# Kernel tuning notes

Measured on AMD Instinct MI355X. Metric: run time of the kernel, lower is better.

## Reference

```python
import jax, jax.numpy as jnp
import numpy as np

DIM = 1024
NUM_HEADS = 16
HEAD_DIM = DIM // NUM_HEADS
ROPE_BASE = 10000.0


def _rope_cos_sin(seq_len, head_dim, dtype):
    inv_freq = 1.0 / (ROPE_BASE ** (jnp.arange(0, head_dim, 2, dtype=jnp.float32) / head_dim))
    t = jnp.arange(seq_len, dtype=jnp.float32)
    freqs = jnp.einsum('i,j->ij', t, inv_freq)          # (S, head_dim/2)
    emb = jnp.concatenate([freqs, freqs], axis=-1)       # (S, head_dim)
    return jnp.cos(emb).astype(dtype), jnp.sin(emb).astype(dtype)


def _rotate_half(x):
    x1, x2 = jnp.split(x, 2, axis=-1)
    return jnp.concatenate([-x2, x1], axis=-1)


def setup_inputs() -> dict:
    key = jax.random.key(0)
    k1, k2, k3 = jax.random.split(key, 3)
    B, S = 2, 2048
    x = jax.random.normal(k1, (B, S, DIM), dtype=jnp.float32)
    w_qkv = jax.random.normal(k2, (3 * DIM, DIM), dtype=jnp.float32) * (DIM ** -0.5)
    w_out = jax.random.normal(k3, (DIM, DIM), dtype=jnp.float32) * (DIM ** -0.5)
    return {"x": x, "w_qkv": w_qkv, "w_out": w_out}


def reference(x, w_qkv, w_out):
    B, S, _ = x.shape
    scale = HEAD_DIM ** -0.5

    qkv = jnp.einsum('bsd,ed->bse', x, w_qkv)                 # (B, S, 3*DIM)
    qkv = qkv.reshape(B, S, 3, NUM_HEADS, HEAD_DIM)
    qkv = jnp.transpose(qkv, (2, 0, 3, 1, 4))                  # (3, B, H, S, hd)
    Q, K, V = qkv[0], qkv[1], qkv[2]

    cos, sin = _rope_cos_sin(S, HEAD_DIM, x.dtype)             # (S, hd)
    Q = Q * cos + _rotate_half(Q) * sin
    K = K * cos + _rotate_half(K) * sin

    scores = jnp.einsum('bhqd,bhkd->bhqk', Q, K) * scale       # (B, H, S, S)
    causal = jnp.tril(jnp.ones((S, S), dtype=bool))
    scores = jnp.where(causal[None, None], scores, jnp.asarray(-1e9, scores.dtype))
    attn = jax.nn.softmax(scores, axis=-1)

    out = jnp.einsum('bhqk,bhkd->bhqd', attn, V)               # (B, H, S, hd)
    out = jnp.transpose(out, (0, 2, 1, 3)).reshape(B, S, DIM)
    out = jnp.einsum('bsd,ed->bse', out, w_out)
    return out
```

## Files before the change

### kernel.cpp

```cpp
#include <hip/hip_runtime.h>
#include <hip/hip_bf16.h>

#define DIM 1024
#define NHEADS 16
#define HD 64
#define BB 2
#define SS 2048
#define MTOT (BB*SS)
#define SCALE 0.125f
#define QSCALE 0.1803368801111204f

typedef __attribute__((ext_vector_type(8))) short bf16x8;
typedef __attribute__((ext_vector_type(4))) float f32x4;

__device__ __forceinline__ float bf2f(short u) {
  union { float f; unsigned int i; } v;
  v.i = ((unsigned int)(unsigned short)u) << 16;
  return v.f;
}
__device__ __forceinline__ short f2bf(float f) {
  union { float f; unsigned int i; } v; v.f = f;
  unsigned int r = v.i + 0x7fffu + ((v.i >> 16) & 1u);
  return (short)(r >> 16);
}
__device__ __forceinline__ unsigned int cvtpk_bf16(float lo, float hi) {
  unsigned int r;
  asm("v_cvt_pk_bf16_f32 %0, %1, %2" : "=v"(r) : "v"(lo), "v"(hi));
  return r;
}
__device__ __forceinline__ void async_load16(const short* g, short* l) {
  __builtin_amdgcn_global_load_lds(
      (const __attribute__((address_space(1))) unsigned int*)g,
      (__attribute__((address_space(3))) unsigned int*)l, 16, 0, 0);
}

__global__ void cvt3_kernel(const float* __restrict__ a, short* __restrict__ oa, int na,
                            const float* __restrict__ b, short* __restrict__ ob, int nb,
                            const float* __restrict__ c, short* __restrict__ oc, int nc) {
  int stride = gridDim.x * blockDim.x;
  int tot = na + nb + nc;
  for (int q = blockIdx.x * blockDim.x + threadIdx.x; q < tot; q += stride) {
    const float* src; short* dst; int off;
    if (q < na)            { src = a; dst = oa; off = q; }
    else if (q < na + nb)  { src = b; dst = ob; off = q - na; }
    else                   { src = c; dst = oc; off = q - na - nb; }
    float4 v = *(const float4*)(src + (size_t)off * 4);
    short4 o;
    o.x = f2bf(v.x); o.y = f2bf(v.y); o.z = f2bf(v.z); o.w = f2bf(v.w);
    *(short4*)(dst + (size_t)off * 4) = o;
  }
}

__global__ void rope_table_kernel(float* __restrict__ ct, float* __restrict__ st) {
  int i = blockIdx.x * blockDim.x + threadIdx.x;
  if (i >= SS * 32) return;
  int s = i >> 5, j = i & 31;
  float inv = 1.0f / powf(10000.0f, (float)(2 * j) / 64.0f);
  float ang = (float)s * inv;
  ct[i] = cosf(ang);
  st[i] = sinf(ang);
}

template<bool OUT_F32>
__global__ __launch_bounds__(256) void gemm_bt(
    const short* __restrict__ A, const short* __restrict__ B,
    void* __restrict__ C, int M, int N, int K) {
  __shared__ __align__(16) short As[128][32];
  __shared__ __align__(16) short Bs[128][32];
  const int nbx = N >> 7;
  const int chunk = gridDim.x >> 3;
  const int wg = (blockIdx.x & 7) * chunk + (blockIdx.x >> 3);
  const int m0 = (wg / nbx) * 128, n0 = (wg % nbx) * 128;
  const int tid = threadIdx.x;
  const int lane = tid & 63;
  const int wid = tid >> 6;
  const int wm = (wid >> 1) * 64, wn = (wid & 1) * 64;
  const int row = lane & 15, kg = (lane >> 4) * 8;
  const int lrow = lane >> 2;
  const int lcol = (lane & 3) * 8;

  f32x4 acc[4][4];
#pragma unroll
  for (int m = 0; m < 4; m++)
#pragma unroll
    for (int n = 0; n < 4; n++) acc[m][n] = (f32x4){0.f, 0.f, 0.f, 0.f};

  for (int kk = 0; kk < K; kk += 32) {
    __syncthreads();
#pragma unroll
    for (int i = 0; i < 2; i++) {
      int base = i * 64 + wid * 16;
      async_load16(A + (size_t)(m0 + base + lrow) * K + kk + lcol, &As[base][0]);
      async_load16(B + (size_t)(n0 + base + lrow) * K + kk + lcol, &Bs[base][0]);
    }
    __syncthreads();
    bf16x8 af[4], bfr[4];
#pragma unroll
    for (int m = 0; m < 4; m++) af[m] = *(const bf16x8*)(&As[wm + m * 16 + row][kg]);
#pragma unroll
    for (int n = 0; n < 4; n++) bfr[n] = *(const bf16x8*)(&Bs[wn + n * 16 + row][kg]);
#pragma unroll
    for (int m = 0; m < 4; m++)
#pragma unroll
      for (int n = 0; n < 4; n++)
        acc[m][n] = __builtin_amdgcn_mfma_f32_16x16x32_bf16(af[m], bfr[n], acc[m][n], 0, 0, 0);
  }
  const int orow = (lane >> 4) * 4, ocol = lane & 15;
#pragma unroll
  for (int m = 0; m < 4; m++)
#pragma unroll
    for (int n = 0; n < 4; n++)
#pragma unroll
      for (int r = 0; r < 4; r++) {
        int gr = m0 + wm + m * 16 + orow + r;
        int gc = n0 + wn + n * 16 + ocol;
        if (OUT_F32) ((float*)C)[(size_t)gr * N + gc] = acc[m][n][r];
        else         ((short*)C)[(size_t)gr * N + gc] = f2bf(acc[m][n][r]);
      }
}

__global__ __launch_bounds__(256) void ropev_kernel(
    const short* __restrict__ qkv, const float* __restrict__ ct, const float* __restrict__ st,
    short* __restrict__ Q, short* __restrict__ K, short* __restrict__ Vt) {
  int bh = blockIdx.y;
  int b = bh >> 4, h = bh & 15;
  int t = threadIdx.x;
  if (blockIdx.x < SS / 64) {
    int s0 = blockIdx.x * 64;
    int rl = t >> 2;
    int d8 = (t & 3) * 8;
    int s = s0 + rl;
    size_t inbase = ((size_t)(b * SS + s)) * 3072 + h * 64 + d8;
    size_t outbase = ((size_t)bh * SS + s) * 64 + d8;
    float c[8], sn[8];
#pragma unroll
    for (int j = 0; j < 8; j++) { c[j] = ct[s * 32 + d8 + j]; sn[j] = st[s * 32 + d8 + j]; }
    {
      bf16x8 x1 = *(const bf16x8*)(qkv + inbase);
      bf16x8 x2 = *(const bf16x8*)(qkv + inbase + 32);
      bf16x8 o1, o2;
#pragma unroll
      for (int j = 0; j < 8; j++) {
        float a = bf2f(x1[j]), bb = bf2f(x2[j]);
        o1[j] = f2bf((a * c[j] - bb * sn[j]) * QSCALE);
        o2[j] = f2bf((bb * c[j] + a * sn[j]) * QSCALE);
      }
      *(bf16x8*)(Q + outbase) = o1;
      *(bf16x8*)(Q + outbase + 32) = o2;
    }
    {
      bf16x8 x1 = *(const bf16x8*)(qkv + inbase + 1024);
      bf16x8 x2 = *(const bf16x8*)(qkv + inbase + 1024 + 32);
      bf16x8 o1, o2;
#pragma unroll
      for (int j = 0; j < 8; j++) {
        float a = bf2f(x1[j]), bb = bf2f(x2[j]);
        o1[j] = f2bf(a * c[j] - bb * sn[j]);
        o2[j] = f2bf(bb * c[j] + a * sn[j]);
      }
      *(bf16x8*)(K + outbase) = o1;
      *(bf16x8*)(K + outbase + 32) = o2;
    }
  } else {
    __shared__ short ls[64][72];
    int s0 = (blockIdx.x - SS / 64) * 64;
#pragma unroll
    for (int p = 0; p < 2; p++) {
      int idx = p * 256 + t;
      int r = idx >> 3, c8 = (idx & 7) * 8;
      *(bf16x8*)(&ls[r][c8]) =
          *(const bf16x8*)(qkv + ((size_t)(b * SS + s0 + r)) * 3072 + 2048 + h * 64 + c8);
    }
    __syncthreads();
    int dl = t >> 2, sg = (t & 3) * 16;
    int c = sg >> 5, hi = (sg >> 4) & 1;
    short tmp[16];
#pragma unroll
    for (int j = 0; j < 16; j++) tmp[j] = ls[sg + j][dl];
    size_t rowbase = ((size_t)bh * 64 + dl) * SS + s0;
#pragma unroll
    for (int g = 0; g < 4; g++) {
      short4 o = { tmp[4 * g], tmp[4 * g + 1], tmp[4 * g + 2], tmp[4 * g + 3] };
      *(short4*)(Vt + rowbase + c * 32 + g * 8 + hi * 4) = o;
    }
  }
}

__global__ __launch_bounds__(256) void attn_kernel(
    const short* __restrict__ Qp, const short* __restrict__ Kp, const short* __restrict__ Vt,
    short* __restrict__ O) {
  __shared__ short Ks[2][64][72];
  __shared__ short Vs[2][64][72];
  int flat = blockIdx.x;
  int wk = (flat & 7) * 64 + (flat >> 3);
  int bh = wk >> 4;
  int pr = wk & 15;
  int b = bh >> 4, h = bh & 15;
  int tid = threadIdx.x, lane = tid & 63, w = tid >> 6;
  int row = lane & 15, grp = lane >> 4;

  const int ksr = tid >> 3;
  const int ksc = (tid & 7) * 8;
  const short* Kbase = Kp + (size_t)bh * SS * 64;
  const short* Vbase = Vt + (size_t)bh * 64 * SS;

  bf16x8 kr0, kr1, vr0, vr1;
  auto LOADT = [&](int kv0) {
    kr0 = *(const bf16x8*)(Kbase + (size_t)(kv0 + ksr) * 64 + ksc);
    kr1 = *(const bf16x8*)(Kbase + (size_t)(kv0 + 32 + ksr) * 64 + ksc);
    vr0 = *(const bf16x8*)(Vbase + (size_t)ksr * SS + kv0 + ksc);
    vr1 = *(const bf16x8*)(Vbase + (size_t)(32 + ksr) * SS + kv0 + ksc);
  };
  auto WRITET = [&](int bufi) {
    *(bf16x8*)(&Ks[bufi][ksr][ksc]) = kr0;
    *(bf16x8*)(&Ks[bufi][32 + ksr][ksc]) = kr1;
    *(bf16x8*)(&Vs[bufi][ksr][ksc]) = vr0;
    *(bf16x8*)(&Vs[bufi][32 + ksr][ksc]) = vr1;
  };

  int cur = 0;
  LOADT(0);
  WRITET(0);
  __syncthreads();

#pragma unroll 1
  for (int s = 0; s < 2; s++) {
    const int qt = s ? pr : 31 - pr;
    const int q0 = qt * 64;
    const int q = q0 + w * 16 + row;
    bf16x8 qf0, qf1;
    {
      size_t qb = ((size_t)bh * SS + q) * 64 + grp * 8;
      qf0 = *(const bf16x8*)(Qp + qb);
      qf1 = *(const bf16x8*)(Qp + qb + 32);
    }
    f32x4 acc[4];
#pragma unroll
    for (int d = 0; d < 4; d++) acc[d] = (f32x4){0.f, 0.f, 0.f, 0.f};
    float m = -1e30f, l = 0.f;

#pragma unroll 1
    for (int kt = 0; kt <= qt; kt++) {
      int kv0 = kt * 64;
      bool more = (kt < qt) || (s == 0);
      if (more) LOADT(kt < qt ? kv0 + 64 : 0);

      bool last = (kt == qt);
      float sv[4][4];
#pragma unroll
      for (int n = 0; n < 4; n++) {
        if (last && n > w) {
#pragma unroll
          for (int r = 0; r < 4; r++) sv[n][r] = -1e30f;
          continue;
        }
        f32x4 sf = (f32x4){0.f, 0.f, 0.f, 0.f};
        bf16x8 kf0 = *(const bf16x8*)(&Ks[cur][n * 16 + row][grp * 8]);
        bf16x8 kf1 = *(const bf16x8*)(&Ks[cur][n * 16 + row][grp * 8 + 32]);
        sf = __builtin_amdgcn_mfma_f32_16x16x32_bf16(kf0, qf0, sf, 0, 0, 0);
        sf = __builtin_amdgcn_mfma_f32_16x16x32_bf16(kf1, qf1, sf, 0, 0, 0);
#pragma unroll
        for (int r = 0; r < 4; r++) sv[n][r] = sf[r];
      }
      if (last) {
#pragma unroll
        for (int n = 0; n < 4; n++)
#pragma unroll
          for (int r = 0; r < 4; r++) {
            int kv = kv0 + n * 16 + grp * 4 + r;
            if (kv > q) sv[n][r] = -1e30f;
          }
      }
      float pmax = -1e30f;
#pragma unroll
      for (int n = 0; n < 4; n++)
#pragma unroll
        for (int r = 0; r < 4; r++) pmax = fmaxf(pmax, sv[n][r]);
      pmax = fmaxf(pmax, __shfl_xor(pmax, 16));
      pmax = fmaxf(pmax, __shfl_xor(pmax, 32));
      float mnew = fmaxf(m, pmax);
      float resc = __builtin_amdgcn_exp2f(m - mnew);
      m = mnew;
      float p[4][4];
      float psum = 0.f;
#pragma unroll
      for (int n = 0; n < 4; n++)
#pragma unroll
        for (int r = 0; r < 4; r++) {
          p[n][r] = __builtin_amdgcn_exp2f(sv[n][r] - m);
          psum += p[n][r];
        }
      psum += __shfl_xor(psum, 16);
      psum += __shfl_xor(psum, 32);
      l = l * resc + psum;
#pragma unroll
      for (int d = 0; d < 4; d++)
#pragma unroll
        for (int r = 0; r < 4; r++) acc[d][r] *= resc;
#pragma unroll
      for (int c = 0; c < 2; c++) {
        union { unsigned int u[4]; bf16x8 v; } pu;
        pu.u[0] = cvtpk_bf16(p[2 * c][0], p[2 * c][1]);
        pu.u[1] = cvtpk_bf16(p[2 * c][2], p[2 * c][3]);
        pu.u[2] = cvtpk_bf16(p[2 * c + 1][0], p[2 * c + 1][1]);
        pu.u[3] = cvtpk_bf16(p[2 * c + 1][2], p[2 * c + 1][3]);
#pragma unroll
        for (int dm = 0; dm < 4; dm++) {
          bf16x8 vf = *(const bf16x8*)(&Vs[cur][dm * 16 + row][c * 32 + grp * 8]);
          acc[dm] = __builtin_amdgcn_mfma_f32_16x16x32_bf16(vf, pu.v, acc[dm], 0, 0, 0);
        }
      }
      if (more) WRITET(cur ^ 1);
      __syncthreads();
      cur ^= 1;
    }
    float linv = 1.0f / l;
    size_t ob = ((size_t)(b * SS + q)) * 1024 + h * 64 + grp * 4;
#pragma unroll
    for (int dm = 0; dm < 4; dm++) {
      union { unsigned int u[2]; short4 s4; } ou;
      ou.u[0] = cvtpk_bf16(acc[dm][0] * linv, acc[dm][1] * linv);
      ou.u[1] = cvtpk_bf16(acc[dm][2] * linv, acc[dm][3] * linv);
      *(short4*)(O + ob + dm * 16) = ou.s4;
    }
  }
}

extern "C" void kernel_launch(void* const* d_in, const int* in_sizes, int n_in,
                              void* d_out, int out_size, void* d_ws, size_t ws_size,
                              hipStream_t stream) {
  (void)in_sizes; (void)n_in; (void)out_size; (void)ws_size;
  const float* x     = (const float*)d_in[0];
  const float* w_qkv = (const float*)d_in[1];
  const float* w_out = (const float*)d_in[2];
  float* out = (float*)d_out;

  char* ws = (char*)d_ws;
  size_t off = 0;
  auto alloc = [&](size_t bytes) -> void* {
    void* p = ws + off;
    off += (bytes + 255) & ~(size_t)255;
    return p;
  };
  short* xb    = (short*)alloc((size_t)MTOT * DIM * 2);
  short* wqkvb = (short*)alloc((size_t)3072 * 1024 * 2);
  short* woutb = (short*)alloc((size_t)1024 * 1024 * 2);
  short* qkvb  = (short*)alloc((size_t)MTOT * 3072 * 2);
  short* Qb    = (short*)alloc((size_t)32 * SS * 64 * 2);
  short* Kb    = (short*)alloc((size_t)32 * SS * 64 * 2);
  short* Vtb   = (short*)alloc((size_t)32 * 64 * SS * 2);
  float* ct    = (float*)alloc((size_t)SS * 32 * 4);
  float* st    = (float*)alloc((size_t)SS * 32 * 4);
  short* attnb = xb;

  cvt3_kernel<<<2048, 256, 0, stream>>>(x, xb, MTOT * DIM / 4,
                                        w_qkv, wqkvb, 3072 * 1024 / 4,
                                        w_out, woutb, 1024 * 1024 / 4);
  rope_table_kernel<<<SS * 32 / 256, 256, 0, stream>>>(ct, st);
  gemm_bt<false><<<(3072 / 128) * (MTOT / 128), 256, 0, stream>>>(xb, wqkvb, qkvb, MTOT, 3072, 1024);
  ropev_kernel<<<dim3(2 * SS / 64, 32), 256, 0, stream>>>(qkvb, ct, st, Qb, Kb, Vtb);
  attn_kernel<<<512, 256, 0, stream>>>(Qb, Kb, Vtb, attnb);
  gemm_bt<true><<<(1024 / 128) * (MTOT / 128), 256, 0, stream>>>(attnb, woutb, out, MTOT, 1024, 1024);
}
```

Baseline: 137.2 us.

## Split attention KV range across two blocks, stage GEMM epilogue, lazy rescale

Attention now launches 1024 blocks. The long query tile of each pair is split across two blocks by KV range, and a new merge kernel combines the partial (acc, m, l) results written to scratch that reuses the qkv buffer. This targets load imbalance and low occupancy, at the cost of an extra launch and extra global traffic. Online softmax rescaling is skipped unless the max grows by more than 8 in log2 space. Separately, the GEMM epilogue is staged through shared memory so stores are row-contiguous vectors instead of scattered scalar writes.

```diff
diff --git a/kernel.cpp b/kernel.cpp
--- a/kernel.cpp
+++ b/kernel.cpp
@@ -65,8 +65,9 @@
 __global__ __launch_bounds__(256) void gemm_bt(
     const short* __restrict__ A, const short* __restrict__ B,
     void* __restrict__ C, int M, int N, int K) {
-  __shared__ __align__(16) short As[128][32];
-  __shared__ __align__(16) short Bs[128][32];
+  __shared__ __align__(16) char smem[16384];
+  auto As = reinterpret_cast<short(*)[32]>(smem);
+  auto Bs = reinterpret_cast<short(*)[32]>(smem + 8192);
   const int nbx = N >> 7;
   const int chunk = gridDim.x >> 3;
   const int wg = (blockIdx.x & 7) * chunk + (blockIdx.x >> 3);
@@ -105,18 +106,37 @@
       for (int n = 0; n < 4; n++)
         acc[m][n] = __builtin_amdgcn_mfma_f32_16x16x32_bf16(af[m], bfr[n], acc[m][n], 0, 0, 0);
   }
+  float* Lf = (float*)smem;
   const int orow = (lane >> 4) * 4, ocol = lane & 15;
-#pragma unroll
-  for (int m = 0; m < 4; m++)
+  const int half = wid >> 1;
+  const int erow = tid >> 3;
+  const int ec = (tid & 7) * 4;
+  const int gr_b = m0 + (erow >> 4) * 64 + (erow & 15);
+#pragma unroll
+  for (int mseg = 0; mseg < 4; mseg++) {
+    __syncthreads();
+    int rL = half * 16 + orow;
 #pragma unroll
     for (int n = 0; n < 4; n++)
 #pragma unroll
-      for (int r = 0; r < 4; r++) {
-        int gr = m0 + wm + m * 16 + orow + r;
-        int gc = n0 + wn + n * 16 + ocol;
-        if (OUT_F32) ((float*)C)[(size_t)gr * N + gc] = acc[m][n][r];
-        else         ((short*)C)[(size_t)gr * N + gc] = f2bf(acc[m][n][r]);
-      }
+      for (int r = 0; r < 4; r++)
+        Lf[(rL + r) * 128 + wn + n * 16 + ocol] = acc[mseg][n][r];
+    __syncthreads();
+    int gr = gr_b + mseg * 16;
+#pragma unroll
+    for (int j = 0; j < 4; j++) {
+      float4 v = *(const float4*)&Lf[erow * 128 + ec + j * 32];
+      int gc = n0 + ec + j * 32;
+      if (OUT_F32) {
+        *(float4*)((float*)C + (size_t)gr * N + gc) = v;
+      } else {
+        union { unsigned int u[2]; short4 s4; } ou;
+        ou.u[0] = cvtpk_bf16(v.x, v.y);
+        ou.u[1] = cvtpk_bf16(v.z, v.w);
+        *(short4*)((short*)C + (size_t)gr * N + gc) = ou.s4;
+      }
+    }
+  }
 }
 
 __global__ __launch_bounds__(256) void ropev_kernel(
@@ -188,16 +208,19 @@
 
 __global__ __launch_bounds__(256) void attn_kernel(
     const short* __restrict__ Qp, const short* __restrict__ Kp, const short* __restrict__ Vt,
-    short* __restrict__ O) {
+    short* __restrict__ O, float* __restrict__ Pf) {
   __shared__ short Ks[2][64][72];
   __shared__ short Vs[2][64][72];
   int flat = blockIdx.x;
-  int wk = (flat & 7) * 64 + (flat >> 3);
-  int bh = wk >> 4;
-  int pr = wk & 15;
+  int wk = (flat & 7) * 128 + (flat >> 3);
+  int bh = wk >> 5;
+  int sub = wk & 31;
+  int pr = sub >> 1, half = sub & 1;
   int b = bh >> 4, h = bh & 15;
   int tid = threadIdx.x, lane = tid & 63, w = tid >> 6;
   int row = lane & 15, grp = lane >> 4;
+  const int qtH = 31 - pr;
+  const int nseg = 1 + half;
 
   const int ksr = tid >> 3;
   const int ksc = (tid & 7) * 8;
@@ -218,14 +241,18 @@
     *(bf16x8*)(&Vs[bufi][32 + ksr][ksc]) = vr1;
   };
 
+  const int kts0 = half ? 16 : 0;
   int cur = 0;
-  LOADT(0);
+  LOADT(kts0 * 64);
   WRITET(0);
   __syncthreads();
 
 #pragma unroll 1
-  for (int s = 0; s < 2; s++) {
-    const int qt = s ? pr : 31 - pr;
+  for (int s = 0; s < nseg; s++) {
+    const int qt  = (s == 0) ? qtH : pr;
+    const int kts = (s == 0) ? kts0 : 0;
+    const int kte = (s == 0) ? (half ? qtH : 15) : pr;
+    const bool fin = (s == 1);
     const int q0 = qt * 64;
     const int q = q0 + w * 16 + row;
     bf16x8 qf0, qf1;
@@ -240,10 +267,10 @@
     float m = -1e30f, l = 0.f;
 
 #pragma unroll 1
-    for (int kt = 0; kt <= qt; kt++) {
+    for (int kt = kts; kt <= kte; kt++) {
       int kv0 = kt * 64;
-      bool more = (kt < qt) || (s == 0);
-      if (more) LOADT(kt < qt ? kv0 + 64 : 0);
+      bool more = (kt < kte) || (s + 1 < nseg);
+      if (more) LOADT(kt < kte ? kv0 + 64 : 0);
 
       bool last = (kt == qt);
       float sv[4][4];
@@ -278,9 +305,16 @@
         for (int r = 0; r < 4; r++) pmax = fmaxf(pmax, sv[n][r]);
       pmax = fmaxf(pmax, __shfl_xor(pmax, 16));
       pmax = fmaxf(pmax, __shfl_xor(pmax, 32));
-      float mnew = fmaxf(m, pmax);
-      float resc = __builtin_amdgcn_exp2f(m - mnew);
-      m = mnew;
+      if (__any(pmax - m > 8.f)) {
+        float mnew = fmaxf(m, pmax);
+        float resc = __builtin_amdgcn_exp2f(m - mnew);
+        m = mnew;
+        l *= resc;
+#pragma unroll
+        for (int d = 0; d < 4; d++)
+#pragma unroll
+          for (int r = 0; r < 4; r++) acc[d][r] *= resc;
+      }
       float p[4][4];
       float psum = 0.f;
 #pragma unroll
@@ -292,11 +326,7 @@
         }
       psum += __shfl_xor(psum, 16);
       psum += __shfl_xor(psum, 32);
-      l = l * resc + psum;
-#pragma unroll
-      for (int d = 0; d < 4; d++)
-#pragma unroll
-        for (int r = 0; r < 4; r++) acc[d][r] *= resc;
+      l += psum;
 #pragma unroll
       for (int c = 0; c < 2; c++) {
         union { unsigned int u[4]; bf16x8 v; } pu;
@@ -314,15 +344,55 @@
       __syncthreads();
       cur ^= 1;
     }
-    float linv = 1.0f / l;
-    size_t ob = ((size_t)(b * SS + q)) * 1024 + h * 64 + grp * 4;
-#pragma unroll
-    for (int dm = 0; dm < 4; dm++) {
-      union { unsigned int u[2]; short4 s4; } ou;
-      ou.u[0] = cvtpk_bf16(acc[dm][0] * linv, acc[dm][1] * linv);
-      ou.u[1] = cvtpk_bf16(acc[dm][2] * linv, acc[dm][3] * linv);
-      *(short4*)(O + ob + dm * 16) = ou.s4;
-    }
+    if (fin) {
+      float linv = 1.0f / l;
+      size_t ob = ((size_t)(b * SS + q)) * 1024 + h * 64 + grp * 4;
+#pragma unroll
+      for (int dm = 0; dm < 4; dm++) {
+        union { unsigned int u[2]; short4 s4; } ou;
+        ou.u[0] = cvtpk_bf16(acc[dm][0] * linv, acc[dm][1] * linv);
+        ou.u[1] = cvtpk_bf16(acc[dm][2] * linv, acc[dm][3] * linv);
+        *(short4*)(O + ob + dm * 16) = ou.s4;
+      }
+    } else {
+      int slot = (bh * 16 + (qt - 16)) * 2 + half;
+      float* P = Pf + (size_t)slot * 64 * 68 + (w * 16 + row) * 68;
+#pragma unroll
+      for (int dm = 0; dm < 4; dm++) {
+        f32x4 a = acc[dm];
+        *(float4*)(P + dm * 16 + grp * 4) = *(float4*)&a;
+      }
+      if (grp == 0) { P[64] = m; P[65] = l; }
+    }
+  }
+}
+
+__global__ __launch_bounds__(64) void merge_kernel(const float* __restrict__ Pf, short* __restrict__ O) {
+  int bh = blockIdx.x >> 4, ht = blockIdx.x & 15;
+  int b = bh >> 4, h = bh & 15;
+  int qt = ht + 16;
+  int t = threadIdx.x;
+  const float* p0 = Pf + ((size_t)((bh * 16 + ht) * 2)) * 64 * 68 + t * 68;
+  const float* p1 = p0 + 64 * 68;
+  float m0 = p0[64], l0 = p0[65], m1 = p1[64], l1 = p1[65];
+  float mM = fmaxf(m0, m1);
+  float e0 = __builtin_amdgcn_exp2f(m0 - mM);
+  float e1 = __builtin_amdgcn_exp2f(m1 - mM);
+  float linv = 1.0f / (e0 * l0 + e1 * l1);
+  size_t ob = ((size_t)(b * SS + qt * 64 + t)) * 1024 + h * 64;
+#pragma unroll
+  for (int d8 = 0; d8 < 8; d8++) {
+    float4 a0 = *(const float4*)(p0 + d8 * 8);
+    float4 a1 = *(const float4*)(p1 + d8 * 8);
+    float4 b0 = *(const float4*)(p0 + d8 * 8 + 4);
+    float4 b1 = *(const float4*)(p1 + d8 * 8 + 4);
+    union { unsigned int u[4]; short4 s4[2]; } ou;
+    ou.u[0] = cvtpk_bf16((e0 * a0.x + e1 * a1.x) * linv, (e0 * a0.y + e1 * a1.y) * linv);
+    ou.u[1] = cvtpk_bf16((e0 * a0.z + e1 * a1.z) * linv, (e0 * a0.w + e1 * a1.w) * linv);
+    ou.u[2] = cvtpk_bf16((e0 * b0.x + e1 * b1.x) * linv, (e0 * b0.y + e1 * b1.y) * linv);
+    ou.u[3] = cvtpk_bf16((e0 * b0.z + e1 * b1.z) * linv, (e0 * b0.w + e1 * b1.w) * linv);
+    *(short4*)(O + ob + d8 * 8) = ou.s4[0];
+    *(short4*)(O + ob + d8 * 8 + 4) = ou.s4[1];
   }
 }
 
@@ -352,6 +422,7 @@
   float* ct    = (float*)alloc((size_t)SS * 32 * 4);
   float* st    = (float*)alloc((size_t)SS * 32 * 4);
   short* attnb = xb;
+  float* Pf    = (float*)qkvb;
 
   cvt3_kernel<<<2048, 256, 0, stream>>>(x, xb, MTOT * DIM / 4,
                                         w_qkv, wqkvb, 3072 * 1024 / 4,
@@ -359,6 +430,7 @@
   rope_table_kernel<<<SS * 32 / 256, 256, 0, stream>>>(ct, st);
   gemm_bt<false><<<(3072 / 128) * (MTOT / 128), 256, 0, stream>>>(xb, wqkvb, qkvb, MTOT, 3072, 1024);
   ropev_kernel<<<dim3(2 * SS / 64, 32), 256, 0, stream>>>(qkvb, ct, st, Qb, Kb, Vtb);
-  attn_kernel<<<512, 256, 0, stream>>>(Qb, Kb, Vtb, attnb);
+  attn_kernel<<<1024, 256, 0, stream>>>(Qb, Kb, Vtb, attnb, Pf);
+  merge_kernel<<<512, 64, 0, stream>>>(Pf, attnb);
   gemm_bt<true><<<(1024 / 128) * (MTOT / 128), 256, 0, stream>>>(attnb, woutb, out, MTOT, 1024, 1024);
 }
```

Result: no change. 139.1 us (+1.4%).
